# Performance work log

Hardware: AMD Instinct MI355X
Metric: run time of the kernel (lower is better)

The kernel has to match this reference:

```python
import jax, jax.numpy as jnp
import numpy as np

HEAD_NUM = 16
NEG_BIG = -2.0**32 + 1.0


def _pos_encoding(T, D):
    pos = np.arange(T)[:, None].astype(np.float64)
    i = np.arange(D)[None, :].astype(np.float64)
    angle = pos / np.power(10000.0, 2.0 * i / D)
    pe = np.empty((T, D), dtype=np.float64)
    pe[:, 0::2] = np.sin(angle[:, 0::2])
    pe[:, 1::2] = np.cos(angle[:, 1::2])
    return jnp.asarray(pe * (D ** 0.5), dtype=jnp.float32)  # scale=True


def setup_inputs() -> dict:
    key = jax.random.key(0)
    ks = jax.random.split(key, 9)
    B, T, D = 32, 512, 1024
    return {
        "queries": jax.random.normal(ks[0], (B, T, D), jnp.float32),
        "keys": jax.random.normal(ks[1], (B, T, D), jnp.float32),
        "query_masks": jax.random.randint(ks[2], (B, 1), 1, T + 1, jnp.int32),
        "key_masks": jax.random.randint(ks[3], (B, 1), 1, T + 1, jnp.int32),
        "W_Query": jax.random.normal(ks[4], (D, D), jnp.float32) * 0.02,
        "W_key": jax.random.normal(ks[5], (D, D), jnp.float32) * 0.02,
        "W_Value": jax.random.normal(ks[6], (D, D), jnp.float32) * 0.02,
        "fw1": jax.random.normal(ks[7], (D, 4 * D), jnp.float32) * 0.02,
        "fw2": jax.random.normal(ks[8], (4 * D, D), jnp.float32) * 0.02,
    }


def reference(queries, keys, query_masks, key_masks, W_Query, W_key, W_Value, fw1, fw2):
    B, T, D = queries.shape
    h = HEAD_NUM
    d = D // h
    pe = _pos_encoding(T, D)  # [T, D]

    # faithful to source: queries get PE; keys = PE(queries_with_PE) (keys input unused)
    q_pe = queries + pe[None]
    k_pe = q_pe + pe[None]

    qs = jnp.einsum('btd,de->bte', q_pe, W_Query)
    ks_ = jnp.einsum('btd,de->bte', k_pe, W_key)
    vs = jnp.einsum('btd,de->bte', ks_, W_Value)  # faithful: values from projected keys

    def split_heads(x):  # [B,T,h*d] -> [h,B,T,d] (matches tf.split/concat on axis 0)
        return x.reshape(B, T, h, d).transpose(2, 0, 1, 3)

    q4, k4, v4 = split_heads(qs), split_heads(ks_), split_heads(vs)

    scores = jnp.einsum('hbqd,hbkd->hbqk', q4, k4) / (d ** 0.5)

    pos = jnp.arange(T)
    km = (pos[None, :] < key_masks).astype(jnp.float32)    # [B,T]
    qm = (pos[None, :] < query_masks).astype(jnp.float32)  # [B,T]

    scores = jnp.where(km[None, :, None, :] == 1.0, scores, NEG_BIG)
    scores = scores - jnp.max(scores, axis=-1, keepdims=True)
    attn = jax.nn.softmax(scores, axis=-1)
    attn = attn * qm[None, :, :, None]

    out = jnp.einsum('hbqk,hbkd->hbqd', attn, v4)
    result = out.transpose(1, 2, 0, 3).reshape(B, T, D)  # merge heads (head-major)

    result = result + q_pe  # use_res
    # feed forward (use_layer_norm=False, no dropout at inference)
    hmid = jax.nn.relu(jnp.einsum('btd,df->btf', result, fw1))
    result = result + jnp.einsum('btf,fd->btd', hmid, fw2)

    # output_type == 'mean'
    return jnp.mean(result, axis=1, keepdims=True)  # [B,1,D]
```

## Files before the change

kernel.cpp:

```cpp
#include <hip/hip_runtime.h>

constexpr int B_  = 32;
constexpr int T_  = 512;
constexpr int D_  = 1024;
constexpr int NH_ = 16;
constexpr int DH_ = 64;
constexpr int F_  = 4096;
constexpr int BT_ = B_ * T_;

typedef __attribute__((ext_vector_type(8))) short bf16x8;
typedef __attribute__((ext_vector_type(4))) float f32x4;

#define DEVI __device__ __forceinline__

DEVI unsigned short f2bf(float f) {
  union { float f; unsigned u; } uf; uf.f = f;
  unsigned r = uf.u + 0x7fffu + ((uf.u >> 16) & 1u);
  return (unsigned short)(r >> 16);
}
DEVI float b2f(unsigned short h) {
  union { unsigned u; float f; } uf; uf.u = ((unsigned)h) << 16;
  return uf.f;
}
DEVI void gload16(const void* g, void* l) {
  __builtin_amdgcn_global_load_lds(
      (const __attribute__((address_space(1))) void*)(uintptr_t)g,
      (__attribute__((address_space(3))) void*)(unsigned)(uintptr_t)l, 16, 0, 0);
}

__global__ void pack_kernel(const float* __restrict__ q,
                            unsigned short* __restrict__ q_pe, unsigned short* __restrict__ k_pe) {
  long i = ((long)blockIdx.x * 256 + threadIdx.x) * 4;
  const float4 qv = *(const float4*)(q + i);
  int t = (int)((i >> 10) & 511);
  int j0 = (int)(i & 1023);
  float pvv[4];
#pragma unroll
  for (int u = 0; u < 4; u++) {
    int j = j0 + u;
    float inv = exp2f(-(2.0f * (float)j / 1024.0f) * 13.2877123795494f);
    float ang = (float)t * inv;
    pvv[u] = ((j & 1) ? cosf(ang) : sinf(ang)) * 32.0f;
  }
  ushort4 a, b;
  a.x = f2bf(qv.x + pvv[0]); a.y = f2bf(qv.y + pvv[1]);
  a.z = f2bf(qv.z + pvv[2]); a.w = f2bf(qv.w + pvv[3]);
  b.x = f2bf(qv.x + 2.f * pvv[0]); b.y = f2bf(qv.y + 2.f * pvv[1]);
  b.z = f2bf(qv.z + 2.f * pvv[2]); b.w = f2bf(qv.w + 2.f * pvv[3]);
  *(ushort4*)(q_pe + i) = a;
  *(ushort4*)(k_pe + i) = b;
}

__global__ void prep_w(const float* __restrict__ Wq, const float* __restrict__ Wk,
                       const float* __restrict__ Wv, const float* __restrict__ fw1,
                       unsigned short* __restrict__ Wqt, unsigned short* __restrict__ Wkt,
                       unsigned short* __restrict__ Wvt, unsigned short* __restrict__ fw1t,
                       unsigned short* __restrict__ Wkbf) {
  const int z = blockIdx.z;
  if (z < 3 && blockIdx.x >= 32) return;
  const float* W = (z == 0) ? Wq : (z == 1) ? Wk : (z == 2) ? Wv : fw1;
  unsigned short* Wt = (z == 0) ? Wqt : (z == 1) ? Wkt : (z == 2) ? Wvt : fw1t;
  const int N = (z == 3) ? F_ : D_;
  __shared__ float tile[32][33];
  int tx = threadIdx.x & 31, ty = threadIdx.x >> 5;
  int bx = blockIdx.x, by = blockIdx.y;
  for (int i = 0; i < 4; i++) {
    int r = by * 32 + ty + i * 8;
    float v = W[(long)r * N + bx * 32 + tx];
    tile[ty + i * 8][tx] = v;
    if (z == 1) Wkbf[(long)r * D_ + bx * 32 + tx] = f2bf(v);
  }
  __syncthreads();
  for (int i = 0; i < 4; i++) {
    int r = bx * 32 + ty + i * 8;
    Wt[(long)r * D_ + by * 32 + tx] = f2bf(tile[tx][ty + i * 8]);
  }
}

template <int EPI>
__global__ __launch_bounds__(256) void gemm_bt(
    const unsigned short* __restrict__ A0, const unsigned short* __restrict__ Bt0,
    unsigned short* __restrict__ C0, float* __restrict__ hacc, int M, int N, int K) {
  __shared__ unsigned short As[128 * 32];
  __shared__ unsigned short Bs[128 * 32];
  const unsigned short* A  = A0;
  const unsigned short* Bt = Bt0;
  unsigned short* C        = C0;

  const int tid = threadIdx.x;
  const int lane = tid & 63, w = tid >> 6;
  const int wr = w >> 1, wc = w & 1;
  const int l15 = lane & 15, lhi = lane >> 4;
  const int brow = blockIdx.y * 128, bcol = blockIdx.x * 128;

  f32x4 acc[4][4] = {};
  const int o = tid * 16;
  const int srow = o >> 6;
  const int skel = (o & 63) >> 1;

  for (int kk = 0; kk < K; kk += 32) {
    gload16(A + (long)(brow + srow) * K + kk + skel,        (char*)As + o);
    gload16(A + (long)(brow + srow + 64) * K + kk + skel,   (char*)As + o + 4096);
    gload16(Bt + (long)(bcol + srow) * K + kk + skel,       (char*)Bs + o);
    gload16(Bt + (long)(bcol + srow + 64) * K + kk + skel,  (char*)Bs + o + 4096);
    __syncthreads();
    bf16x8 af[4], bfr[4];
    for (int m = 0; m < 4; m++)
      af[m] = *(const bf16x8*)((const char*)As + ((wr * 64 + m * 16 + l15) * 64 + lhi * 16));
    for (int n = 0; n < 4; n++)
      bfr[n] = *(const bf16x8*)((const char*)Bs + ((wc * 64 + n * 16 + l15) * 64 + lhi * 16));
    for (int m = 0; m < 4; m++)
      for (int n = 0; n < 4; n++)
        acc[m][n] = __builtin_amdgcn_mfma_f32_16x16x32_bf16(af[m], bfr[n], acc[m][n], 0, 0, 0);
    __syncthreads();
  }

  for (int m = 0; m < 4; m++)
    for (int n = 0; n < 4; n++) {
      int row = brow + wr * 64 + m * 16 + lhi * 4;
      int col = bcol + wc * 64 + n * 16 + l15;
      for (int r = 0; r < 4; r++)
        C[(long)(row + r) * N + col] = f2bf(acc[m][n][r]);
    }
}

template <int EPI>
__global__ __launch_bounds__(512, 2) void gemm8(
    const unsigned short* __restrict__ A0, const unsigned short* __restrict__ Bt0, unsigned short* __restrict__ C0,
    const unsigned short* __restrict__ A1, const unsigned short* __restrict__ Bt1, unsigned short* __restrict__ C1,
    const unsigned short* __restrict__ A2, const unsigned short* __restrict__ Bt2, unsigned short* __restrict__ C2,
    float* __restrict__ hacc, int N,
    const int* __restrict__ L0, const int* __restrict__ L1, const int* __restrict__ L2) {
  constexpr int K = 1024, NK = 16, NI = 8;
  __shared__ char lds[2][2][32768];

  const int z = blockIdx.z;
  const unsigned short* A  = (z == 0) ? A0  : (z == 1 ? A1  : A2);
  const unsigned short* Bt = (z == 0) ? Bt0 : (z == 1 ? Bt1 : Bt2);
  unsigned short* C        = (z == 0) ? C0  : (z == 1 ? C1  : C2);
  const int* L             = (z == 0) ? L0  : (z == 1 ? L1  : L2);

  const long brow = (long)blockIdx.x * 256, bcol = (long)blockIdx.y * 256;
  if (L && (brow & 256) && L[brow >> 9] <= 256) return;

  const int tid = threadIdx.x;
  const int lane = tid & 63, w = tid >> 6;
  const int wm = w >> 2, wn = w & 3;
  const int l15 = lane & 15, lhi = lane >> 4;

  const int drow = (tid * 16) >> 7;
  const int dcol = ((tid * 16) & 127) ^ ((drow & 7) << 4);
  const int sw   = (l15 & 7) << 4;

  f32x4 acc[8][4] = {};
  bf16x8 bfr[4][2], af[2][2];

  auto STAGE = [&](const unsigned short* __restrict__ P, long tb, int kt, int h, int buf, int op) {
    const unsigned short* g = P + (tb + h * 128 + drow) * (long)K + kt * 64 + (dcol >> 1);
    char* l = &lds[buf][op][h * 16384 + tid * 16];
    gload16(g, l);
    gload16(g + 64L * K, l + 8192);
  };
  auto LDA = [&](int buf, int q) {
#pragma unroll
    for (int mi = 0; mi < 2; mi++) {
      int row = wm * 128 + (q * 2 + mi) * 16 + l15;
#pragma unroll
      for (int kk = 0; kk < 2; kk++)
        af[mi][kk] = *(const bf16x8*)(&lds[buf][0][0] + (row << 7) + ((kk * 64 + lhi * 16) ^ sw));
    }
  };
  auto LDB = [&](int buf) {
#pragma unroll
    for (int n = 0; n < 4; n++) {
      int row = wn * 64 + n * 16 + l15;
#pragma unroll
      for (int kk = 0; kk < 2; kk++)
        bfr[n][kk] = *(const bf16x8*)(&lds[buf][1][0] + (row << 7) + ((kk * 64 + lhi * 16) ^ sw));
    }
  };
  auto MFMAQ = [&](int q) {
    __builtin_amdgcn_s_setprio(1);
#pragma unroll
    for (int mi = 0; mi < 2; mi++)
#pragma unroll
      for (int n = 0; n < 4; n++)
#pragma unroll
        for (int kk = 0; kk < 2; kk++)
          acc[q * 2 + mi][n] =
              __builtin_amdgcn_mfma_f32_16x16x32_bf16(af[mi][kk], bfr[n][kk], acc[q * 2 + mi][n], 0, 0, 0);
    __builtin_amdgcn_s_setprio(0);
  };
#define BAR() __builtin_amdgcn_s_barrier()
#define GATE4() asm volatile("s_waitcnt vmcnt(4)" ::: "memory")

  STAGE(A, brow, 0, 0, 0, 0);  STAGE(A, brow, 0, 1, 0, 0);
  STAGE(Bt, bcol, 0, 0, 0, 1); STAGE(Bt, bcol, 0, 1, 0, 1);
  STAGE(Bt, bcol, 1, 0, 1, 1); STAGE(Bt, bcol, 1, 1, 1, 1);
  GATE4();
  BAR();

  for (int i = 0; i < NI; ++i) {
    const int k1 = 2 * i + 1;
    const int ka = (2 * i + 2) & (NK - 1);
    const int kb = (2 * i + 3) & (NK - 1);
    LDA(0, 0); LDB(0); STAGE(A, brow, k1, 0, 1, 0);
    BAR(); MFMAQ(0); BAR();
    LDA(0, 1);         STAGE(A, brow, k1, 1, 1, 0);
    BAR(); MFMAQ(1); BAR();
    LDA(0, 2);         STAGE(Bt, bcol, ka, 0, 0, 1);
    BAR(); MFMAQ(2); BAR();
    LDA(0, 3);         STAGE(Bt, bcol, ka, 1, 0, 1);
    BAR(); MFMAQ(3);
    GATE4();
    BAR();
    LDA(1, 0); LDB(1); STAGE(A, brow, ka, 0, 0, 0);
    BAR(); MFMAQ(0); BAR();
    LDA(1, 1);         STAGE(A, brow, ka, 1, 0, 0);
    BAR(); MFMAQ(1); BAR();
    LDA(1, 2);         STAGE(Bt, bcol, kb, 0, 1, 1);
    BAR(); MFMAQ(2); BAR();
    LDA(1, 3);         STAGE(Bt, bcol, kb, 1, 1, 1);
    BAR(); MFMAQ(3);
    GATE4();
    BAR();
  }
#undef BAR
#undef GATE4

  if (EPI == 0) {
    if (z == 2) {
      asm volatile("s_waitcnt vmcnt(0)" ::: "memory");
      __builtin_amdgcn_s_barrier();
      char* tl = &lds[0][0][0] + (w << 14);
#pragma unroll
      for (int m = 0; m < 8; m++)
#pragma unroll
        for (int n = 0; n < 4; n++) {
          int cl = n * 16 + l15;
#pragma unroll
          for (int r = 0; r < 4; r++) {
            int tofs = m * 16 + lhi * 4 + r;
            *(unsigned short*)(tl + cl * 256 + ((tofs * 2) ^ ((cl & 7) << 4))) = f2bf(acc[m][n][r]);
          }
        }
      asm volatile("" ::: "memory");
      const int bb = (int)(brow >> 9), t0 = (int)(brow & 511);
#pragma unroll
      for (int rr = 0; rr < 16; rr++) {
        int row = rr * 4 + lhi;
        bf16x8 v = *(const bf16x8*)(tl + row * 256 + ((l15 * 16) ^ ((row & 7) << 4)));
        int gcol = (int)bcol + wn * 64 + row;
        long vtrow = ((long)(bb * NH_ + (gcol >> 6))) * DH_ + (gcol & 63);
        *(bf16x8*)(C + vtrow * T_ + t0 + wm * 128 + l15 * 8) = v;
      }
    } else {
#pragma unroll
      for (int m = 0; m < 8; m++)
#pragma unroll
        for (int n = 0; n < 4; n++) {
          long row = brow + wm * 128 + m * 16 + lhi * 4;
          long col = bcol + wn * 64 + n * 16 + l15;
#pragma unroll
          for (int r = 0; r < 4; r++)
            C[(row + r) * (long)N + col] = f2bf(acc[m][n][r]);
        }
    }
  } else {
    const int batch = (int)(brow >> 9);
#pragma unroll
    for (int n = 0; n < 4; n++) {
      float t = 0.f;
#pragma unroll
      for (int m = 0; m < 8; m++)
#pragma unroll
        for (int r = 0; r < 4; r++) t += fmaxf(acc[m][n][r], 0.f);
      t += __shfl_xor(t, 16);
      t += __shfl_xor(t, 32);
      if (lane < 16)
        atomicAdd(hacc + (long)batch * F_ + bcol + wn * 64 + n * 16 + l15, t);
    }
  }
}

__global__ __launch_bounds__(256, 3) void attn_kernel(
    const unsigned short* __restrict__ qs, const unsigned short* __restrict__ ks,
    const unsigned short* __restrict__ vt, const unsigned short* __restrict__ q_pe,
    const int* __restrict__ qmask, const int* __restrict__ kmask,
    unsigned short* __restrict__ res, float* __restrict__ racc) {
  __shared__ unsigned short Ks[2][64 * 64];
  __shared__ unsigned short Vs[2][64 * 64];
  __shared__ unsigned short Ps[4][32 * 64];

  const int tid = threadIdx.x, lane = tid & 63, w = tid >> 6;
  const int l15 = lane & 15, lhi = lane >> 4;
  const int h = blockIdx.x, b = blockIdx.y, q0 = blockIdx.z * 128;
  const int qlen = qmask[b], kvlen = kmask[b];

  if (q0 >= qlen) {
    int cc = tid & 63;
    float s = 0.f;
    for (int i = 0; i < 32; i++) {
      int r = (tid >> 6) * 32 + i;
      long addr = (long)(b * T_ + q0 + r) * D_ + h * DH_ + cc;
      unsigned short v = q_pe[addr];
      res[addr] = v;
      s += b2f(v);
    }
    atomicAdd(racc + b * D_ + h * DH_ + cc, s);
    return;
  }

  bf16x8 qf[2][2];
  for (int m = 0; m < 2; m++)
    for (int k2 = 0; k2 < 2; k2++) {
      int t = q0 + w * 32 + m * 16 + l15;
      qf[m][k2] = *(const bf16x8*)(qs + (long)(b * T_ + t) * D_ + h * DH_ + k2 * 32 + lhi * 8);
    }

  f32x4 o[2][4] = {};
  float mrun[2][4], lrun[2][4];
  for (int m = 0; m < 2; m++)
    for (int r = 0; r < 4; r++) { mrun[m][r] = -3e38f; lrun[m][r] = 0.f; }

  const float SCL = 0.125f * 1.4426950408889634f;
  const float THR = 8.0f / SCL;
  const int nc = (kvlen + 63) >> 6;

  auto stage = [&](int c, int buf) {
#pragma unroll
    for (int cl = 0; cl < 2; cl++) {
      int ob = cl * 4096 + tid * 16;
      int os = ob ^ (((ob >> 7) & 7) << 4);
      int r0 = os >> 7, cb = os & 127;
      gload16(ks + (long)(b * T_ + c * 64 + r0) * D_ + h * DH_ + (cb >> 1),
              (char*)&Ks[buf][0] + ob);
      gload16(vt + ((long)(b * NH_ + h) * DH_ + r0) * T_ + c * 64 + (cb >> 1),
              (char*)&Vs[buf][0] + ob);
    }
  };

  stage(0, 0);
  int cur = 0;
  for (int c = 0; c < nc; c++) {
    const int nxt = (c + 1 < nc) ? c + 1 : c;
    stage(nxt, cur ^ 1);
    asm volatile("s_waitcnt vmcnt(4)" ::: "memory");
    __builtin_amdgcn_sched_barrier(0);
    __builtin_amdgcn_s_barrier();

    f32x4 s[2][4] = {};
    for (int k2 = 0; k2 < 2; k2++)
      for (int n = 0; n < 4; n++) {
        int key = n * 16 + l15;
        int Ab = key * 128 + (k2 * 32 + lhi * 8) * 2;
        bf16x8 kf = *(const bf16x8*)((const char*)&Ks[cur][0] + (Ab ^ ((key & 7) << 4)));
        s[0][n] = __builtin_amdgcn_mfma_f32_16x16x32_bf16(qf[0][k2], kf, s[0][n], 0, 0, 0);
        s[1][n] = __builtin_amdgcn_mfma_f32_16x16x32_bf16(qf[1][k2], kf, s[1][n], 0, 0, 0);
      }

    if (c == nc - 1) {
      for (int n = 0; n < 4; n++)
        if (c * 64 + n * 16 + l15 >= kvlen)
          for (int m = 0; m < 2; m++) s[m][n] = f32x4{-3e38f, -3e38f, -3e38f, -3e38f};
    }

    for (int m = 0; m < 2; m++) {
      float mx[4];
      for (int r = 0; r < 4; r++) {
        float v = s[m][0][r];
        for (int n = 1; n < 4; n++) v = fmaxf(v, s[m][n][r]);
        mx[r] = v;
      }
      for (int msk = 1; msk < 16; msk <<= 1)
        for (int r = 0; r < 4; r++) mx[r] = fmaxf(mx[r], __shfl_xor(mx[r], msk));
      bool grow = false;
      for (int r = 0; r < 4; r++) grow = grow || (mx[r] > mrun[m][r] + THR);
      if (__any(grow)) {
        float corr[4];
        for (int r = 0; r < 4; r++) {
          float mn = fmaxf(mrun[m][r], mx[r]);
          corr[r] = exp2f((mrun[m][r] - mn) * SCL);
          mrun[m][r] = mn;
        }
        for (int nd = 0; nd < 4; nd++)
          for (int r = 0; r < 4; r++) o[m][nd][r] *= corr[r];
        for (int r = 0; r < 4; r++) lrun[m][r] *= corr[r];
      }
      float ps[4] = {0.f, 0.f, 0.f, 0.f};
      for (int n = 0; n < 4; n++)
        for (int r = 0; r < 4; r++) {
          float pval = exp2f((s[m][n][r] - mrun[m][r]) * SCL);
          s[m][n][r] = pval;
          ps[r] += pval;
        }
      for (int msk = 1; msk < 16; msk <<= 1)
        for (int r = 0; r < 4; r++) ps[r] += __shfl_xor(ps[r], msk);
      for (int r = 0; r < 4; r++) lrun[m][r] += ps[r];
      for (int n = 0; n < 4; n++)
        for (int r = 0; r < 4; r++) {
          int row = m * 16 + lhi * 4 + r;
          int Ab = row * 128 + (n * 16 + l15) * 2;
          *(unsigned short*)((char*)&Ps[w][0] + (Ab ^ ((row & 7) << 4))) = f2bf(s[m][n][r]);
        }
    }
    asm volatile("" ::: "memory");

    for (int k4 = 0; k4 < 2; k4++) {
      bf16x8 pa[2];
      for (int m = 0; m < 2; m++) {
        int row = m * 16 + l15;
        int Ab = row * 128 + k4 * 64 + lhi * 16;
        pa[m] = *(const bf16x8*)((const char*)&Ps[w][0] + (Ab ^ ((row & 7) << 4)));
      }
      for (int nd = 0; nd < 4; nd++) {
        int dv = nd * 16 + l15;
        int Ab = dv * 128 + k4 * 64 + lhi * 16;
        bf16x8 vb = *(const bf16x8*)((const char*)&Vs[cur][0] + (Ab ^ ((dv & 7) << 4)));
        for (int m = 0; m < 2; m++)
          o[m][nd] = __builtin_amdgcn_mfma_f32_16x16x32_bf16(pa[m], vb, o[m][nd], 0, 0, 0);
      }
    }
    __builtin_amdgcn_s_barrier();
    cur ^= 1;
  }

  float cs[4] = {0.f, 0.f, 0.f, 0.f};
  for (int m = 0; m < 2; m++)
    for (int r = 0; r < 4; r++) {
      int t = q0 + w * 32 + m * 16 + lhi * 4 + r;
      float inv = 1.0f / lrun[m][r];
      bool valid = t < qlen;
      for (int nd = 0; nd < 4; nd++) {
        long addr = (long)(b * T_ + t) * D_ + h * DH_ + nd * 16 + l15;
        float v = valid ? o[m][nd][r] * inv : 0.f;
        float val = v + b2f(q_pe[addr]);
        res[addr] = f2bf(val);
        cs[nd] += val;
      }
    }
  for (int nd = 0; nd < 4; nd++) {
    cs[nd] += __shfl_xor(cs[nd], 16);
    cs[nd] += __shfl_xor(cs[nd], 32);
  }
  if (lane < 16)
    for (int nd = 0; nd < 4; nd++)
      atomicAdd(racc + b * D_ + h * DH_ + nd * 16 + l15, cs[nd]);
}

__global__ void final_kernel(const float* __restrict__ hacc, const float* __restrict__ fw2,
                             const float* __restrict__ racc, float* __restrict__ out) {
  int n = blockIdx.x * 64 + (threadIdx.x & 63);
  int bg = threadIdx.x >> 6;
  int f0 = blockIdx.y * 512;
  float acc[8] = {};
  for (int f = f0; f < f0 + 512; f++) {
    float wv = fw2[(long)f * D_ + n];
    for (int i = 0; i < 8; i++) acc[i] += hacc[(long)(bg * 8 + i) * F_ + f] * wv;
  }
  if (blockIdx.y == 0)
    for (int i = 0; i < 8; i++) acc[i] += racc[(long)(bg * 8 + i) * D_ + n];
  for (int i = 0; i < 8; i++)
    atomicAdd(out + (bg * 8 + i) * D_ + n, acc[i] * (1.0f / 512.0f));
}

extern "C" void kernel_launch(void* const* d_in, const int* in_sizes, int n_in,
                              void* d_out, int out_size, void* d_ws, size_t ws_size,
                              hipStream_t stream) {
  const float* queries = (const float*)d_in[0];
  const int*   qmask = (const int*)d_in[2];
  const int*   kmask = (const int*)d_in[3];
  const float* Wq  = (const float*)d_in[4];
  const float* Wk  = (const float*)d_in[5];
  const float* Wv  = (const float*)d_in[6];
  const float* fw1 = (const float*)d_in[7];
  const float* fw2 = (const float*)d_in[8];
  float* out = (float*)d_out;

  char* p = (char*)d_ws;
  auto alloc = [&](size_t bytes) -> char* {
    char* r = p; p += (bytes + 255) & ~(size_t)255; return r;
  };
  unsigned short* q_pe = (unsigned short*)alloc((size_t)BT_ * D_ * 2);
  unsigned short* k_pe = (unsigned short*)alloc((size_t)BT_ * D_ * 2);
  unsigned short* qs   = (unsigned short*)alloc((size_t)BT_ * D_ * 2);
  unsigned short* ksb  = (unsigned short*)alloc((size_t)BT_ * D_ * 2);
  unsigned short* vt   = (unsigned short*)alloc((size_t)BT_ * D_ * 2);
  unsigned short* res  = (unsigned short*)alloc((size_t)BT_ * D_ * 2);
  unsigned short* Wqt  = (unsigned short*)alloc((size_t)D_ * D_ * 2);
  unsigned short* Wkt  = (unsigned short*)alloc((size_t)D_ * D_ * 2);
  unsigned short* Wvt  = (unsigned short*)alloc((size_t)D_ * D_ * 2);
  unsigned short* Wkbf = (unsigned short*)alloc((size_t)D_ * D_ * 2);
  unsigned short* Wkvt = (unsigned short*)alloc((size_t)D_ * D_ * 2);
  unsigned short* fw1t = (unsigned short*)alloc((size_t)D_ * F_ * 2);
  float*          racc = (float*)alloc((size_t)B_ * D_ * 4);
  float*          hacc = (float*)alloc((size_t)B_ * F_ * 4);

  hipMemsetAsync(hacc, 0, (size_t)B_ * F_ * 4, stream);
  hipMemsetAsync(racc, 0, (size_t)B_ * D_ * 4, stream);
  hipMemsetAsync(out, 0, (size_t)B_ * D_ * 4, stream);

  pack_kernel<<<BT_ * D_ / 1024, 256, 0, stream>>>(queries, q_pe, k_pe);
  prep_w<<<dim3(128, 32, 4), 256, 0, stream>>>(Wq, Wk, Wv, fw1, Wqt, Wkt, Wvt, fw1t, Wkbf);

  gemm_bt<0><<<dim3(8, 8, 1), 256, 0, stream>>>(Wvt, Wkbf, Wkvt, nullptr, D_, D_, D_);

  gemm8<0><<<dim3(64, 4, 3), 512, 0, stream>>>(q_pe, Wqt, qs,
                                               k_pe, Wkt, ksb,
                                               k_pe, Wkvt, vt,
                                               nullptr, D_, qmask, kmask, kmask);

  attn_kernel<<<dim3(16, 32, 4), 256, 0, stream>>>(qs, ksb, vt, q_pe, qmask, kmask, res, racc);

  gemm8<1><<<dim3(64, 16, 1), 512, 0, stream>>>(res, fw1t, nullptr,
                                                res, fw1t, nullptr,
                                                res, fw1t, nullptr,
                                                hacc, F_, nullptr, nullptr, nullptr);

  final_kernel<<<dim3(16, 8), 256, 0, stream>>>(hacc, fw2, racc, out);
}
```

Baseline: 409.7 us.

## Run FFN first GEMM in FP8 with scaled MX MFMA

```diff
diff --git a/kernel.cpp b/kernel.cpp
--- a/kernel.cpp
+++ b/kernel.cpp
@@ -10,6 +10,7 @@
 
 typedef __attribute__((ext_vector_type(8))) short bf16x8;
 typedef __attribute__((ext_vector_type(4))) float f32x4;
+typedef __attribute__((ext_vector_type(8))) int i32x8;
 
 #define DEVI __device__ __forceinline__
 
@@ -22,10 +23,20 @@
   union { unsigned u; float f; } uf; uf.u = ((unsigned)h) << 16;
   return uf.f;
 }
+DEVI unsigned char f2fp8(float f) {
+  return (unsigned char)(__builtin_amdgcn_cvt_pk_fp8_f32(f, f, 0, false) & 0xFF);
+}
 DEVI void gload16(const void* g, void* l) {
   __builtin_amdgcn_global_load_lds(
       (const __attribute__((address_space(1))) void*)(uintptr_t)g,
       (__attribute__((address_space(3))) void*)(unsigned)(uintptr_t)l, 16, 0, 0);
+}
+DEVI i32x8 ld32(const char* p0, const char* p1) {
+  int4 lo = *(const int4*)p0, hi = *(const int4*)p1;
+  i32x8 r;
+  r[0] = lo.x; r[1] = lo.y; r[2] = lo.z; r[3] = lo.w;
+  r[4] = hi.x; r[5] = hi.y; r[6] = hi.z; r[7] = hi.w;
+  return r;
 }
 
 __global__ void pack_kernel(const float* __restrict__ q,
@@ -54,12 +65,12 @@
 __global__ void prep_w(const float* __restrict__ Wq, const float* __restrict__ Wk,
                        const float* __restrict__ Wv, const float* __restrict__ fw1,
                        unsigned short* __restrict__ Wqt, unsigned short* __restrict__ Wkt,
-                       unsigned short* __restrict__ Wvt, unsigned short* __restrict__ fw1t,
+                       unsigned short* __restrict__ Wvt, unsigned char* __restrict__ fw1t8,
                        unsigned short* __restrict__ Wkbf) {
   const int z = blockIdx.z;
   if (z < 3 && blockIdx.x >= 32) return;
   const float* W = (z == 0) ? Wq : (z == 1) ? Wk : (z == 2) ? Wv : fw1;
-  unsigned short* Wt = (z == 0) ? Wqt : (z == 1) ? Wkt : (z == 2) ? Wvt : fw1t;
+  unsigned short* Wt = (z == 0) ? Wqt : (z == 1) ? Wkt : Wvt;
   const int N = (z == 3) ? F_ : D_;
   __shared__ float tile[32][33];
   int tx = threadIdx.x & 31, ty = threadIdx.x >> 5;
@@ -73,7 +84,8 @@
   __syncthreads();
   for (int i = 0; i < 4; i++) {
     int r = bx * 32 + ty + i * 8;
-    Wt[(long)r * D_ + by * 32 + tx] = f2bf(tile[tx][ty + i * 8]);
+    if (z == 3) fw1t8[(long)r * D_ + by * 32 + tx] = f2fp8(tile[tx][ty + i * 8] * 64.0f);
+    else        Wt[(long)r * D_ + by * 32 + tx] = f2bf(tile[tx][ty + i * 8]);
   }
 }
 
@@ -283,11 +295,114 @@
   }
 }
 
+__global__ __launch_bounds__(512, 2) void gemmf8(
+    const unsigned char* __restrict__ A, const unsigned char* __restrict__ Bt,
+    float* __restrict__ hacc) {
+  constexpr int K = 1024, NKT = 8, NI = 4;
+  __shared__ char lds[2][2][32768];
+  const long brow = (long)blockIdx.x * 256, bcol = (long)blockIdx.y * 256;
+  const int tid = threadIdx.x;
+  const int lane = tid & 63, w = tid >> 6;
+  const int wm = w >> 2, wn = w & 3;
+  const int l15 = lane & 15, lhi = lane >> 4;
+
+  const int drow = (tid * 16) >> 7;
+  const int dcol = ((tid * 16) & 127) ^ ((drow & 7) << 4);
+  const int sw   = (l15 & 7) << 4;
+
+  f32x4 acc[8][4] = {};
+  i32x8 af[2], bfr[4];
+
+  auto STAGE = [&](const unsigned char* __restrict__ P, long tb, int kt, int h, int buf, int op) {
+    const unsigned char* g = P + (tb + h * 128 + drow) * (long)K + kt * 128 + dcol;
+    char* l = &lds[buf][op][h * 16384 + tid * 16];
+    gload16(g, l);
+    gload16(g + 64L * K, l + 8192);
+  };
+  auto LDA = [&](int buf, int q) {
+#pragma unroll
+    for (int mi = 0; mi < 2; mi++) {
+      int row = wm * 128 + (q * 2 + mi) * 16 + l15;
+      const char* base = &lds[buf][0][0] + (row << 7);
+      af[mi] = ld32(base + ((lhi * 32) ^ sw), base + ((lhi * 32 + 16) ^ sw));
+    }
+  };
+  auto LDB = [&](int buf) {
+#pragma unroll
+    for (int n = 0; n < 4; n++) {
+      int row = wn * 64 + n * 16 + l15;
+      const char* base = &lds[buf][1][0] + (row << 7);
+      bfr[n] = ld32(base + ((lhi * 32) ^ sw), base + ((lhi * 32 + 16) ^ sw));
+    }
+  };
+  auto MFMAQ = [&](int q) {
+    __builtin_amdgcn_s_setprio(1);
+#pragma unroll
+    for (int mi = 0; mi < 2; mi++)
+#pragma unroll
+      for (int n = 0; n < 4; n++)
+        acc[q * 2 + mi][n] = __builtin_amdgcn_mfma_scale_f32_16x16x128_f8f6f4(
+            af[mi], bfr[n], acc[q * 2 + mi][n], 0, 0,
+            0, 0x7F7F7F7F, 0, 0x7F7F7F7F);
+    __builtin_amdgcn_s_setprio(0);
+  };
+#define BAR() __builtin_amdgcn_s_barrier()
+#define GATE4() asm volatile("s_waitcnt vmcnt(4)" ::: "memory")
+
+  STAGE(A, brow, 0, 0, 0, 0);  STAGE(A, brow, 0, 1, 0, 0);
+  STAGE(Bt, bcol, 0, 0, 0, 1); STAGE(Bt, bcol, 0, 1, 0, 1);
+  STAGE(Bt, bcol, 1, 0, 1, 1); STAGE(Bt, bcol, 1, 1, 1, 1);
+  GATE4();
+  BAR();
+
+  for (int i = 0; i < NI; ++i) {
+    const int k1 = 2 * i + 1;
+    const int ka = (2 * i + 2) & (NKT - 1);
+    const int kb = (2 * i + 3) & (NKT - 1);
+    LDA(0, 0); LDB(0); STAGE(A, brow, k1, 0, 1, 0);
+    BAR(); MFMAQ(0); BAR();
+    LDA(0, 1);         STAGE(A, brow, k1, 1, 1, 0);
+    BAR(); MFMAQ(1); BAR();
+    LDA(0, 2);         STAGE(Bt, bcol, ka, 0, 0, 1);
+    BAR(); MFMAQ(2); BAR();
+    LDA(0, 3);         STAGE(Bt, bcol, ka, 1, 0, 1);
+    BAR(); MFMAQ(3);
+    GATE4();
+    BAR();
+    LDA(1, 0); LDB(1); STAGE(A, brow, ka, 0, 0, 0);
+    BAR(); MFMAQ(0); BAR();
+    LDA(1, 1);         STAGE(A, brow, ka, 1, 0, 0);
+    BAR(); MFMAQ(1); BAR();
+    LDA(1, 2);         STAGE(Bt, bcol, kb, 0, 1, 1);
+    BAR(); MFMAQ(2); BAR();
+    LDA(1, 3);         STAGE(Bt, bcol, kb, 1, 1, 1);
+    BAR(); MFMAQ(3);
+    GATE4();
+    BAR();
+  }
+#undef BAR
+#undef GATE4
+
+  const int batch = (int)(brow >> 9);
+#pragma unroll
+  for (int n = 0; n < 4; n++) {
+    float t = 0.f;
+#pragma unroll
+    for (int m = 0; m < 8; m++)
+#pragma unroll
+      for (int r = 0; r < 4; r++) t += fmaxf(acc[m][n][r], 0.f);
+    t += __shfl_xor(t, 16);
+    t += __shfl_xor(t, 32);
+    if (lane < 16)
+      atomicAdd(hacc + (long)batch * F_ + bcol + wn * 64 + n * 16 + l15, t);
+  }
+}
+
 __global__ __launch_bounds__(256, 3) void attn_kernel(
     const unsigned short* __restrict__ qs, const unsigned short* __restrict__ ks,
     const unsigned short* __restrict__ vt, const unsigned short* __restrict__ q_pe,
     const int* __restrict__ qmask, const int* __restrict__ kmask,
-    unsigned short* __restrict__ res, float* __restrict__ racc) {
+    unsigned char* __restrict__ res8, float* __restrict__ racc) {
   __shared__ unsigned short Ks[2][64 * 64];
   __shared__ unsigned short Vs[2][64 * 64];
   __shared__ unsigned short Ps[4][32 * 64];
@@ -303,9 +418,9 @@
     for (int i = 0; i < 32; i++) {
       int r = (tid >> 6) * 32 + i;
       long addr = (long)(b * T_ + q0 + r) * D_ + h * DH_ + cc;
-      unsigned short v = q_pe[addr];
-      res[addr] = v;
-      s += b2f(v);
+      float v = b2f(q_pe[addr]);
+      res8[addr] = f2fp8(v);
+      s += v;
     }
     atomicAdd(racc + b * D_ + h * DH_ + cc, s);
     return;
@@ -435,7 +550,7 @@
         long addr = (long)(b * T_ + t) * D_ + h * DH_ + nd * 16 + l15;
         float v = valid ? o[m][nd][r] * inv : 0.f;
         float val = v + b2f(q_pe[addr]);
-        res[addr] = f2bf(val);
+        res8[addr] = f2fp8(val);
         cs[nd] += val;
       }
     }
@@ -458,10 +573,11 @@
     float wv = fw2[(long)f * D_ + n];
     for (int i = 0; i < 8; i++) acc[i] += hacc[(long)(bg * 8 + i) * F_ + f] * wv;
   }
-  if (blockIdx.y == 0)
-    for (int i = 0; i < 8; i++) acc[i] += racc[(long)(bg * 8 + i) * D_ + n];
-  for (int i = 0; i < 8; i++)
-    atomicAdd(out + (bg * 8 + i) * D_ + n, acc[i] * (1.0f / 512.0f));
+  for (int i = 0; i < 8; i++) {
+    float v = acc[i] * (1.0f / (512.0f * 64.0f));
+    if (blockIdx.y == 0) v += racc[(long)(bg * 8 + i) * D_ + n] * (1.0f / 512.0f);
+    atomicAdd(out + (bg * 8 + i) * D_ + n, v);
+  }
 }
 
 extern "C" void kernel_launch(void* const* d_in, const int* in_sizes, int n_in,
@@ -486,13 +602,13 @@
   unsigned short* qs   = (unsigned short*)alloc((size_t)BT_ * D_ * 2);
   unsigned short* ksb  = (unsigned short*)alloc((size_t)BT_ * D_ * 2);
   unsigned short* vt   = (unsigned short*)alloc((size_t)BT_ * D_ * 2);
-  unsigned short* res  = (unsigned short*)alloc((size_t)BT_ * D_ * 2);
+  unsigned char*  res8 = (unsigned char*)alloc((size_t)BT_ * D_);
   unsigned short* Wqt  = (unsigned short*)alloc((size_t)D_ * D_ * 2);
   unsigned short* Wkt  = (unsigned short*)alloc((size_t)D_ * D_ * 2);
   unsigned short* Wvt  = (unsigned short*)alloc((size_t)D_ * D_ * 2);
   unsigned short* Wkbf = (unsigned short*)alloc((size_t)D_ * D_ * 2);
   unsigned short* Wkvt = (unsigned short*)alloc((size_t)D_ * D_ * 2);
-  unsigned short* fw1t = (unsigned short*)alloc((size_t)D_ * F_ * 2);
+  unsigned char*  fw1t8 = (unsigned char*)alloc((size_t)D_ * F_);
   float*          racc = (float*)alloc((size_t)B_ * D_ * 4);
   float*          hacc = (float*)alloc((size_t)B_ * F_ * 4);
 
@@ -501,7 +617,7 @@
   hipMemsetAsync(out, 0, (size_t)B_ * D_ * 4, stream);
 
   pack_kernel<<<BT_ * D_ / 1024, 256, 0, stream>>>(queries, q_pe, k_pe);
-  prep_w<<<dim3(128, 32, 4), 256, 0, stream>>>(Wq, Wk, Wv, fw1, Wqt, Wkt, Wvt, fw1t, Wkbf);
+  prep_w<<<dim3(128, 32, 4), 256, 0, stream>>>(Wq, Wk, Wv, fw1, Wqt, Wkt, Wvt, fw1t8, Wkbf);
 
   gemm_bt<0><<<dim3(8, 8, 1), 256, 0, stream>>>(Wvt, Wkbf, Wkvt, nullptr, D_, D_, D_);
 
@@ -510,12 +626,9 @@
                                                k_pe, Wkvt, vt,
                                                nullptr, D_, qmask, kmask, kmask);
 
-  attn_kernel<<<dim3(16, 32, 4), 256, 0, stream>>>(qs, ksb, vt, q_pe, qmask, kmask, res, racc);
-
-  gemm8<1><<<dim3(64, 16, 1), 512, 0, stream>>>(res, fw1t, nullptr,
-                                                res, fw1t, nullptr,
-                                                res, fw1t, nullptr,
-                                                hacc, F_, nullptr, nullptr, nullptr);
+  attn_kernel<<<dim3(16, 32, 4), 256, 0, stream>>>(qs, ksb, vt, q_pe, qmask, kmask, res8, racc);
+
+  gemmf8<<<dim3(64, 16), 512, 0, stream>>>(res8, fw1t8, hacc);
 
   final_kernel<<<dim3(16, 8), 256, 0, stream>>>(hacc, fw2, racc, out);
 }
```

Result: no change. 413.7 us (+1.0%).
